# Optimization experiments

Hardware: AMD Instinct MI355X
Metric: run time of the kernel (lower is better)

Reference implementation:

```python
import jax, jax.numpy as jnp
import numpy as np

N_NODES = 20000
N_EDGES = 320000
IN_DIM = 256
HIDDEN = 256
OUT_DIM = 128
N_LAYERS = 3
N_GROUPS = 4
EXP_PER_GROUP = 2
N_EXPERTS = N_GROUPS * EXP_PER_GROUP
TOP_K = 2


def setup_inputs() -> dict:
    key = jax.random.key(0)
    ks = jax.random.split(key, 12)
    d = HIDDEN
    r = 2 * d  # router/expert input dim: concat(node, neighbor-mean)
    x = jax.random.normal(ks[0], (N_NODES, IN_DIM), dtype=jnp.float32)
    edge_index = jax.random.randint(ks[1], (2, N_EDGES), 0, N_NODES, dtype=jnp.int32)
    s = 0.05
    Wg = jax.random.normal(ks[2], (N_LAYERS, r, N_GROUPS), dtype=jnp.float32) * s
    We = jax.random.normal(ks[3], (N_LAYERS, r, N_EXPERTS), dtype=jnp.float32) * s
    Ww = jax.random.normal(ks[4], (N_LAYERS, r, d), dtype=jnp.float32) * s
    W1 = jax.random.normal(ks[5], (N_LAYERS, N_EXPERTS, r, d), dtype=jnp.float32) * s
    b1 = jnp.zeros((N_LAYERS, N_EXPERTS, d), dtype=jnp.float32)
    W2 = jax.random.normal(ks[6], (N_LAYERS, N_EXPERTS, d, d), dtype=jnp.float32) * s
    b2 = jnp.zeros((N_LAYERS, N_EXPERTS, d), dtype=jnp.float32)
    wc = jax.random.normal(ks[7], (N_LAYERS, r, 1), dtype=jnp.float32) * s
    Wout = jax.random.normal(ks[8], (d, OUT_DIM), dtype=jnp.float32) * s
    return {"x": x, "edge_index": edge_index, "Wg": Wg, "We": We, "Ww": Ww,
            "W1": W1, "b1": b1, "W2": W2, "b2": b2, "wc": wc, "Wout": Wout}


def _moe_layer(h, src, dst, deg, Wg, We, Ww, W1, b1, W2, b2, wc):
    N = h.shape[0]
    # graph message passing: mean aggregation over incoming edges
    agg = jax.ops.segment_sum(h[src], dst, num_segments=N) / deg  # [N, d]
    r = jnp.concatenate([h, agg], axis=-1)  # [N, 2d] combined router input
    # hierarchical routing: group softmax x within-group expert softmax
    gp = jax.nn.softmax(r @ Wg, axis=-1)                                # [N, G]
    ep = jax.nn.softmax((r @ We).reshape(N, N_GROUPS, EXP_PER_GROUP), axis=-1)
    probs = (gp[..., None] * ep).reshape(N, N_EXPERTS)                  # [N, E]
    # top-k gating, renormalized
    topv, topi = jax.lax.top_k(probs, TOP_K)
    gates = jnp.zeros_like(probs).at[jnp.arange(N)[:, None], topi].set(topv)
    gates = gates / (gates.sum(-1, keepdims=True) + 1e-9)              # [N, E]
    # strong experts: per-expert 2-layer MLP, combined by gates
    hid = jax.nn.relu(jnp.einsum('nf,efd->ned', r, W1) + b1[None])      # [N, E, d]
    exp_out = jnp.einsum('ned,edo->neo', hid, W2) + b2[None]            # [N, E, d]
    strong = jnp.einsum('ne,neo->no', gates, exp_out)                   # [N, d]
    # weak shared expert + confidence gate blend
    weak = r @ Ww                                                       # [N, d]
    conf = jax.nn.sigmoid(r @ wc)                                       # [N, 1]
    return jax.nn.relu(conf * strong + (1.0 - conf) * weak)


def reference(x, edge_index, Wg, We, Ww, W1, b1, W2, b2, wc, Wout):
    src, dst = edge_index[0], edge_index[1]
    N = x.shape[0]
    deg = jax.ops.segment_sum(jnp.ones((edge_index.shape[1],), jnp.float32), dst,
                              num_segments=N)
    deg = jnp.maximum(deg, 1.0)[:, None]
    h = x
    for l in range(Wg.shape[0]):  # small fixed layer loop
        h = _moe_layer(h, src, dst, deg, Wg[l], We[l], Ww[l],
                       W1[l], b1[l], W2[l], b2[l], wc[l])
    return h @ Wout
```

## Files before the change

### kernel.cpp

```cpp
#include <hip/hip_runtime.h>

#define NN 20000
#define NEDGE 320000
#define D 256
#define RD 512
#define OD 128
#define NEXP 8
#define NSLOT (2*NN)
#define NODE_BLOCKS 79
#define ASSIGN_BLOCKS 157
#define EXP_BLOCKS 640

typedef unsigned short u16;
typedef __attribute__((ext_vector_type(4))) short short4v;
typedef __attribute__((ext_vector_type(8))) short short8v;
typedef __attribute__((ext_vector_type(16))) float f32x16;

__device__ __forceinline__ void split1(float v, u16& h, u16& m, u16& l) {
    unsigned b = __float_as_uint(v);
    h = (u16)(b >> 16);
    float fh = __uint_as_float(b & 0xffff0000u);
    float r1 = v - fh;
    unsigned b1 = __float_as_uint(r1);
    m = (u16)(b1 >> 16);
    float fm = __uint_as_float(b1 & 0xffff0000u);
    float r2 = r1 - fm;
    l = (u16)(__float_as_uint(r2) >> 16);
}


__global__ void copy_x_zero_cnt_k(const float* __restrict__ x, float* __restrict__ r,
                                  int* __restrict__ cnt) {
    int gid = blockIdx.x * 256 + threadIdx.x;
    int n = gid >> 6;
    int c4 = gid & 63;
    if (gid < NN * (D / 4)) {
        float4 v = reinterpret_cast<const float4*>(x)[gid];
        reinterpret_cast<float4*>(r + (size_t)n * RD)[c4] = v;
    }
    if (gid < NN) cnt[gid] = 0;
}

__global__ void count_edges_k(const int* __restrict__ dst, int* __restrict__ cnt) {
    int e = blockIdx.x * 256 + threadIdx.x;
    if (e < NEDGE) atomicAdd(&cnt[dst[e]], 1);
}

__global__ void block_sums_k(const int* __restrict__ cnt, int* __restrict__ bsum) {
    __shared__ int s[256];
    int i = blockIdx.x * 256 + threadIdx.x;
    s[threadIdx.x] = (i < NN) ? cnt[i] : 0;
    __syncthreads();
    for (int off = 128; off > 0; off >>= 1) {
        if (threadIdx.x < off) s[threadIdx.x] += s[threadIdx.x + off];
        __syncthreads();
    }
    if (threadIdx.x == 0) bsum[blockIdx.x] = s[0];
}

__global__ void scan_bsums_k(int* __restrict__ bsum, int* __restrict__ row_start) {
    if (blockIdx.x == 0 && threadIdx.x == 0) {
        int acc = 0;
        for (int i = 0; i < NODE_BLOCKS; i++) { int t = bsum[i]; bsum[i] = acc; acc += t; }
        row_start[NN] = acc;
    }
}

__global__ void block_scan_k(const int* __restrict__ cnt, const int* __restrict__ bsum,
                             int* __restrict__ row_start, int* __restrict__ cur) {
    __shared__ int s[256];
    int i = blockIdx.x * 256 + threadIdx.x;
    int v = (i < NN) ? cnt[i] : 0;
    s[threadIdx.x] = v;
    __syncthreads();
    for (int off = 1; off < 256; off <<= 1) {
        int t = (threadIdx.x >= off) ? s[threadIdx.x - off] : 0;
        __syncthreads();
        s[threadIdx.x] += t;
        __syncthreads();
    }
    int excl = s[threadIdx.x] - v + bsum[blockIdx.x];
    if (i < NN) { row_start[i] = excl; cur[i] = excl; }
}

__global__ void fill_csr_k(const int* __restrict__ src, const int* __restrict__ dst,
                           int* __restrict__ cur, int* __restrict__ csr_src) {
    int e = blockIdx.x * 256 + threadIdx.x;
    if (e < NEDGE) {
        int pos = atomicAdd(&cur[dst[e]], 1);
        csr_src[pos] = src[e];
    }
}

__global__ void zero_k(float* __restrict__ p, int n4) {
    int i = blockIdx.x * 256 + threadIdx.x;
    if (i < n4) reinterpret_cast<float4*>(p)[i] = make_float4(0.f, 0.f, 0.f, 0.f);
}

__global__ void aggregate_k(float* __restrict__ r, const int* __restrict__ row_start,
                            const int* __restrict__ csr_src) {
    int wid = blockIdx.x * 4 + (threadIdx.x >> 6);
    int lane = threadIdx.x & 63;
    if (wid >= NN) return;
    int beg = row_start[wid], end = row_start[wid + 1];
    float ax = 0.f, ay = 0.f, az = 0.f, aw = 0.f;
    for (int j = beg; j < end; j++) {
        int s = csr_src[j];
        float4 v = reinterpret_cast<const float4*>(r + (size_t)s * RD)[lane];
        ax += v.x; ay += v.y; az += v.z; aw += v.w;
    }
    float deg = (float)((end - beg) > 1 ? (end - beg) : 1);
    float4 o = make_float4(ax / deg, ay / deg, az / deg, aw / deg);
    reinterpret_cast<float4*>(r + (size_t)wid * RD + D)[lane] = o;
}

__global__ void router_k(const float* __restrict__ r, const float* __restrict__ Wg,
                         const float* __restrict__ We, const float* __restrict__ wc,
                         int* __restrict__ node_top, float* __restrict__ node_gate,
                         float* __restrict__ conf) {
    int wid = blockIdx.x * 4 + (threadIdx.x >> 6);
    int lane = threadIdx.x & 63;
    if (wid >= NN) return;

    const float* rrow = r + (size_t)wid * RD;
    float pg[4] = {0, 0, 0, 0};
    float pe[8] = {0, 0, 0, 0, 0, 0, 0, 0};
    float pc = 0.f;
#pragma unroll
    for (int i = 0; i < 8; i++) {
        int k = lane + i * 64;
        float rv = rrow[k];
        float4 wg = *reinterpret_cast<const float4*>(Wg + (size_t)k * 4);
        pg[0] = fmaf(rv, wg.x, pg[0]); pg[1] = fmaf(rv, wg.y, pg[1]);
        pg[2] = fmaf(rv, wg.z, pg[2]); pg[3] = fmaf(rv, wg.w, pg[3]);
        float4 w0 = *reinterpret_cast<const float4*>(We + (size_t)k * 8);
        float4 w1 = *reinterpret_cast<const float4*>(We + (size_t)k * 8 + 4);
        pe[0] = fmaf(rv, w0.x, pe[0]); pe[1] = fmaf(rv, w0.y, pe[1]);
        pe[2] = fmaf(rv, w0.z, pe[2]); pe[3] = fmaf(rv, w0.w, pe[3]);
        pe[4] = fmaf(rv, w1.x, pe[4]); pe[5] = fmaf(rv, w1.y, pe[5]);
        pe[6] = fmaf(rv, w1.z, pe[6]); pe[7] = fmaf(rv, w1.w, pe[7]);
        pc = fmaf(rv, wc[k], pc);
    }
#pragma unroll
    for (int off = 32; off > 0; off >>= 1) {
#pragma unroll
        for (int g = 0; g < 4; g++) pg[g] += __shfl_xor(pg[g], off);
#pragma unroll
        for (int g = 0; g < 8; g++) pe[g] += __shfl_xor(pe[g], off);
        pc += __shfl_xor(pc, off);
    }

    if (lane == 0) {
        float m = fmaxf(fmaxf(pg[0], pg[1]), fmaxf(pg[2], pg[3]));
        float eg[4]; float sg = 0.f;
#pragma unroll
        for (int g = 0; g < 4; g++) { eg[g] = expf(pg[g] - m); sg += eg[g]; }
        float probs[8];
#pragma unroll
        for (int g = 0; g < 4; g++) {
            float a = pe[2 * g], b = pe[2 * g + 1];
            float mm = fmaxf(a, b);
            float ea = expf(a - mm), eb = expf(b - mm);
            float inv = 1.f / (ea + eb);
            float gp = eg[g] / sg;
            probs[2 * g]     = gp * ea * inv;
            probs[2 * g + 1] = gp * eb * inv;
        }
        int i0 = 0; float v0 = probs[0];
#pragma unroll
        for (int j = 1; j < 8; j++) if (probs[j] > v0) { v0 = probs[j]; i0 = j; }
        int i1 = -1; float v1 = -1e30f;
#pragma unroll
        for (int j = 0; j < 8; j++) if (j != i0 && probs[j] > v1) { v1 = probs[j]; i1 = j; }
        float s = v0 + v1 + 1e-9f;
        node_top[2 * wid] = i0;  node_top[2 * wid + 1] = i1;
        node_gate[2 * wid] = v0 / s;  node_gate[2 * wid + 1] = v1 / s;
        conf[wid] = 1.f / (1.f + expf(-pc));
    }
}

__global__ void hist_part_k(const int* __restrict__ node_top, int* __restrict__ part) {
    __shared__ int h[NEXP];
    if (threadIdx.x < NEXP) h[threadIdx.x] = 0;
    __syncthreads();
    int i = blockIdx.x * 256 + threadIdx.x;
    if (i < NSLOT) atomicAdd(&h[node_top[i]], 1);
    __syncthreads();
    if (threadIdx.x < NEXP) part[blockIdx.x * NEXP + threadIdx.x] = h[threadIdx.x];
}

__global__ void scan2_k(const int* __restrict__ part, int* __restrict__ es,
                        int* __restrict__ ecur) {
    __shared__ int tot[NEXP];
    if (threadIdx.x < NEXP) {
        int s = 0;
        for (int b = 0; b < ASSIGN_BLOCKS; b++) s += part[b * NEXP + threadIdx.x];
        tot[threadIdx.x] = s;
        ecur[threadIdx.x] = 0;
    }
    __syncthreads();
    if (threadIdx.x == 0) {
        int acc = 0;
        for (int e = 0; e < NEXP; e++) { es[e] = acc; acc += tot[e]; }
        es[NEXP] = acc;
    }
}

__global__ void fill_experts_k(const int* __restrict__ node_top, const float* __restrict__ node_gate,
                               const int* __restrict__ es, int* __restrict__ ecur,
                               int* __restrict__ slot_node, float* __restrict__ slot_gate) {
    __shared__ int hcnt[NEXP], hbase[NEXP];
    int tid = threadIdx.x;
    if (tid < NEXP) hcnt[tid] = 0;
    __syncthreads();
    int i = blockIdx.x * 256 + tid;
    int e = 0, local = 0;
    bool act = (i < NSLOT);
    if (act) {
        e = node_top[i];
        local = atomicAdd(&hcnt[e], 1);
    }
    __syncthreads();
    if (tid < NEXP) hbase[tid] = (hcnt[tid] > 0) ? atomicAdd(&ecur[tid], hcnt[tid]) : 0;
    __syncthreads();
    if (act) {
        int slot = es[e] + hbase[e] + local;
        slot_node[slot] = i >> 1;
        slot_gate[slot] = node_gate[i];
    }
}

__global__ void combine_k(const float* __restrict__ strong, const float* __restrict__ weak,
                          const float* __restrict__ conf, float* __restrict__ r) {
    int gid = blockIdx.x * 256 + threadIdx.x;
    if (gid >= NN * (D / 4)) return;
    int n = gid >> 6, c4 = gid & 63;
    float4 e = reinterpret_cast<const float4*>(strong + (size_t)n * D)[c4];
    float4 w = reinterpret_cast<const float4*>(weak + (size_t)n * D)[c4];
    float cf = conf[n], cg = 1.f - cf;
    float4 o;
    o.x = fmaxf(cf * e.x + cg * w.x, 0.f);
    o.y = fmaxf(cf * e.y + cg * w.y, 0.f);
    o.z = fmaxf(cf * e.z + cg * w.z, 0.f);
    o.w = fmaxf(cf * e.w + cg * w.w, 0.f);
    reinterpret_cast<float4*>(r + (size_t)n * RD)[c4] = o;
}

__device__ __forceinline__ void btile_one(const float* __restrict__ src,
                                          u16* __restrict__ dH, u16* __restrict__ dM,
                                          u16* __restrict__ dL, int K, int N, int gid) {
    int l = gid & 63;
    int tile = gid >> 6;
    int K16 = K >> 4;
    int kb = tile % K16;
    int t2 = tile / K16;
    int N32 = N >> 5;
    int nb = t2 % N32;
    int mat = t2 / N32;
    int kbase = (kb << 4) + ((l >> 5) << 3);
    int n = (nb << 5) + (l & 31);
    const float* s = src + ((size_t)mat * K + kbase) * N + n;
    short8v vh, vm, vl;
#pragma unroll
    for (int j = 0; j < 8; j++) {
        u16 hh, mm, ll;
        split1(s[(size_t)j * N], hh, mm, ll);
        vh[j] = (short)hh; vm[j] = (short)mm; vl[j] = (short)ll;
    }
    size_t o = (size_t)gid * 8;
    *reinterpret_cast<short8v*>(dH + o) = vh;
    *reinterpret_cast<short8v*>(dM + o) = vm;
    *reinterpret_cast<short8v*>(dL + o) = vl;
}

__global__ void btile_k(const float* __restrict__ src, u16* __restrict__ dH,
                        u16* __restrict__ dM, u16* __restrict__ dL,
                        int K, int N, int total) {
    int gid = blockIdx.x * 256 + threadIdx.x;
    if (gid >= total) return;
    btile_one(src, dH, dM, dL, K, N, gid);
}

__global__ void btile3_k(const float* __restrict__ s1, u16* __restrict__ aH,
                         u16* __restrict__ aM, u16* __restrict__ aL,
                         const float* __restrict__ s2, u16* __restrict__ bH,
                         u16* __restrict__ bM, u16* __restrict__ bL,
                         const float* __restrict__ s3, u16* __restrict__ cH,
                         u16* __restrict__ cM, u16* __restrict__ cL) {
    int gid = blockIdx.x * 256 + threadIdx.x;
    if (gid < 131072) {
        btile_one(s1, aH, aM, aL, RD, D, gid);
    } else if (gid < 131072 + 65536) {
        btile_one(s2, bH, bM, bL, D, D, gid - 131072);
    } else if (gid < 131072 + 65536 + 16384) {
        btile_one(s3, cH, cM, cL, RD, D, gid - 131072 - 65536);
    }
}

template <int MODE>
__global__ __launch_bounds__(256, 5) void gemm_mfma(
    const float* __restrict__ A, int lda,
    const u16* __restrict__ BH, const u16* __restrict__ BM,
    const u16* __restrict__ BL,
    const float* __restrict__ bias,
    float* __restrict__ C, int ldc,
    const int* __restrict__ es,
    const int* __restrict__ slot_node,
    const float* __restrict__ slot_gate,
    int M, int N, int K,
    const u16* __restrict__ VH, const u16* __restrict__ VM,
    const u16* __restrict__ VL, float* __restrict__ Cw,
    int weak_base, int Mw) {
    constexpr int PL2 = 1024;
    __shared__ u16 sA[3 * PL2];

    int tid = threadIdx.x;
    int row0, valid_rows;
    bool isweak = false;
    if (MODE == 0) {
        row0 = blockIdx.x * 64;
        valid_rows = M - row0; if (valid_rows > 64) valid_rows = 64;
    } else if (MODE == 1 && (int)blockIdx.x >= weak_base) {
        isweak = true;
        row0 = ((int)blockIdx.x - weak_base) * 64;
        valid_rows = Mw - row0; if (valid_rows > 64) valid_rows = 64;
        if (valid_rows <= 0) return;
        BH = VH; BM = VM; BL = VL;
        C = Cw;
    } else {
        int bx = blockIdx.x, acc0 = 0, expert = -1, mt = 0;
        row0 = 0; valid_rows = 0;
        for (int e = 0; e < NEXP; e++) {
            int c = es[e + 1] - es[e];
            int t = (c + 63) >> 6;
            if (bx < acc0 + t) {
                expert = e; mt = bx - acc0; row0 = es[e] + (mt << 6);
                valid_rows = c - (mt << 6); if (valid_rows > 64) valid_rows = 64;
                break;
            }
            acc0 += t;
        }
        if (expert < 0) return;
        int bo = expert * N * K;
        BH += bo; BM += bo; BL += bo;
        bias += expert * D;
    }
    int ncol0 = blockIdx.y * 128;

    int srow = tid >> 2;
    int koff = (tid & 3) * 4;
    int grow;
    {
        int i0 = row0 + srow;
        if (MODE == 1 && !isweak) {
            i0 = i0 < NSLOT ? i0 : NSLOT - 1;
            grow = slot_node[i0];
        } else if (MODE == 2) {
            grow = i0 < M ? i0 : M - 1;
        } else if (MODE == 1) {
            grow = i0 < Mw ? i0 : Mw - 1;
        } else {
            grow = i0 < M ? i0 : M - 1;
        }
    }
    const float* pA = A + (size_t)grow * lda + koff;
    int woff = ((srow >> 5) * 2 + (koff >> 3)) * 256 + (srow & 31) * 8 + (koff & 4);

    int lane = tid & 63;
    int wave = tid >> 6;
    int wr = (wave & 1) * 32;
    int wc = (wave >> 1) * 64;
    int fl = lane & 31;
    int K16 = K >> 4;
    int nb0 = (ncol0 + wc) >> 5;
    int tbase0 = nb0 * K16 * 512 + lane * 8;
    int tbase1 = (nb0 + 1) * K16 * 512 + lane * 8;
    int roff = ((wr >> 5) * 2 + (lane >> 5)) * 256 + fl * 8;

    f32x16 acc0 = {};
    f32x16 acc1 = {};

    for (int kt = 0; kt < K; kt += 16) {
        float4 av = *reinterpret_cast<const float4*>(pA + kt);
        int ko = (kt >> 4) * 512;
        short8v bH0 = *reinterpret_cast<const short8v*>(BH + tbase0 + ko);
        short8v bM0 = *reinterpret_cast<const short8v*>(BM + tbase0 + ko);
        short8v bL0 = *reinterpret_cast<const short8v*>(BL + tbase0 + ko);
        short8v bH1 = *reinterpret_cast<const short8v*>(BH + tbase1 + ko);
        short8v bM1 = *reinterpret_cast<const short8v*>(BM + tbase1 + ko);
        short8v bL1 = *reinterpret_cast<const short8v*>(BL + tbase1 + ko);
        __syncthreads();
        {
            u16 h0, m0, l0, h1, m1, l1, h2, m2, l2, h3, m3, l3;
            split1(av.x, h0, m0, l0);
            split1(av.y, h1, m1, l1);
            split1(av.z, h2, m2, l2);
            split1(av.w, h3, m3, l3);
            short4v hv = {(short)h0, (short)h1, (short)h2, (short)h3};
            short4v mv = {(short)m0, (short)m1, (short)m2, (short)m3};
            short4v lv = {(short)l0, (short)l1, (short)l2, (short)l3};
            *reinterpret_cast<short4v*>(&sA[0 * PL2 + woff]) = hv;
            *reinterpret_cast<short4v*>(&sA[1 * PL2 + woff]) = mv;
            *reinterpret_cast<short4v*>(&sA[2 * PL2 + woff]) = lv;
        }
        __syncthreads();
        short8v aH = *reinterpret_cast<const short8v*>(&sA[0 * PL2 + roff]);
        short8v aM = *reinterpret_cast<const short8v*>(&sA[1 * PL2 + roff]);
        short8v aL = *reinterpret_cast<const short8v*>(&sA[2 * PL2 + roff]);
#define MFMA_ACC(d, a, b) d = __builtin_amdgcn_mfma_f32_32x32x16_bf16(a, b, d, 0, 0, 0)
        MFMA_ACC(acc0, aH, bH0); MFMA_ACC(acc0, aH, bM0);
        MFMA_ACC(acc0, aM, bH0); MFMA_ACC(acc0, aH, bL0);
        MFMA_ACC(acc0, aM, bM0); MFMA_ACC(acc0, aL, bH0);
        MFMA_ACC(acc1, aH, bH1); MFMA_ACC(acc1, aH, bM1);
        MFMA_ACC(acc1, aM, bH1); MFMA_ACC(acc1, aH, bL1);
        MFMA_ACC(acc1, aM, bM1); MFMA_ACC(acc1, aL, bH1);
#undef MFMA_ACC
    }

    int fh = lane >> 5;
#pragma unroll
    for (int j = 0; j < 2; j++) {
        const f32x16& a = j ? acc1 : acc0;
        int colg = ncol0 + wc + j * 32 + fl;
        float bv = (MODE != 0 && !isweak) ? bias[colg] : 0.f;
#pragma unroll
        for (int rg = 0; rg < 16; rg++) {
            int lrow = wr + (rg & 3) + 8 * (rg >> 2) + 4 * fh;
            if (lrow >= valid_rows) continue;
            int growo = row0 + lrow;
            float v = a[rg] + bv;
            if (MODE == 1 && !isweak) {
                v = fmaxf(v, 0.f);
                C[(size_t)growo * ldc + colg] = v;
            } else if (MODE == 2) {
                v *= slot_gate[growo];
                int node = slot_node[growo];
                atomicAdd(&C[(size_t)node * ldc + colg], v);
            } else {
                C[(size_t)growo * ldc + colg] = v;
            }
        }
    }
}

extern "C" void kernel_launch(void* const* d_in, const int* in_sizes, int n_in,
                              void* d_out, int out_size, void* d_ws, size_t ws_size,
                              hipStream_t stream) {
    (void)in_sizes; (void)n_in; (void)out_size; (void)ws_size;
    const float* x    = (const float*)d_in[0];
    const int*   ei   = (const int*)d_in[1];
    const float* Wg   = (const float*)d_in[2];
    const float* We   = (const float*)d_in[3];
    const float* Ww   = (const float*)d_in[4];
    const float* W1   = (const float*)d_in[5];
    const float* b1   = (const float*)d_in[6];
    const float* W2   = (const float*)d_in[7];
    const float* b2   = (const float*)d_in[8];
    const float* wcp  = (const float*)d_in[9];
    const float* Wout = (const float*)d_in[10];
    float* out = (float*)d_out;

    char* p = (char*)d_ws;
    auto alloc = [&](size_t bytes) -> char* {
        char* q = p; p += (bytes + 255) & ~(size_t)255; return q;
    };
    int*   cnt       = (int*)alloc((size_t)NN * 4);
    int*   row_start = (int*)alloc((size_t)(NN + 1) * 4);
    int*   cur       = (int*)alloc((size_t)NN * 4);
    int*   bsum      = (int*)alloc(128 * 4);
    int*   csr_src   = (int*)alloc((size_t)NEDGE * 4);
    float* r         = (float*)alloc((size_t)NN * RD * 4);
    float* hid       = (float*)alloc((size_t)NSLOT * D * 4);
    float* strong    = (float*)alloc((size_t)NN * D * 4);
    float* weak      = (float*)alloc((size_t)NN * D * 4);
    float* conf      = (float*)alloc((size_t)NN * 4);
    int*   node_top  = (int*)alloc((size_t)2 * NN * 4);
    float* node_gate = (float*)alloc((size_t)2 * NN * 4);
    int*   slot_node = (int*)alloc((size_t)NSLOT * 4);
    float* slot_gate = (float*)alloc((size_t)NSLOT * 4);
    int*   part      = (int*)alloc((size_t)ASSIGN_BLOCKS * NEXP * 4);
    int*   es        = (int*)alloc(64 * 4);
    int*   ecur      = (int*)alloc(64 * 4);
    u16* w1tH = (u16*)alloc((size_t)NEXP * D * RD * 2);
    u16* w1tM = (u16*)alloc((size_t)NEXP * D * RD * 2);
    u16* w1tL = (u16*)alloc((size_t)NEXP * D * RD * 2);
    u16* w2tH = (u16*)alloc((size_t)NEXP * D * D * 2);
    u16* w2tM = (u16*)alloc((size_t)NEXP * D * D * 2);
    u16* w2tL = (u16*)alloc((size_t)NEXP * D * D * 2);
    u16* wwtH = (u16*)alloc((size_t)D * RD * 2);
    u16* wwtM = (u16*)alloc((size_t)D * RD * 2);
    u16* wwtL = (u16*)alloc((size_t)D * RD * 2);
    u16* wotH = (u16*)alloc((size_t)OD * D * 2);
    u16* wotM = (u16*)alloc((size_t)OD * D * 2);
    u16* wotL = (u16*)alloc((size_t)OD * D * 2);

    const int* srcp = ei;
    const int* dstp = ei + NEDGE;
    const int EB = (NEDGE + 255) / 256;

    copy_x_zero_cnt_k<<<5000, 256, 0, stream>>>(x, r, cnt);
    count_edges_k<<<EB, 256, 0, stream>>>(dstp, cnt);
    block_sums_k<<<NODE_BLOCKS, 256, 0, stream>>>(cnt, bsum);
    scan_bsums_k<<<1, 64, 0, stream>>>(bsum, row_start);
    block_scan_k<<<NODE_BLOCKS, 256, 0, stream>>>(cnt, bsum, row_start, cur);
    fill_csr_k<<<EB, 256, 0, stream>>>(srcp, dstp, cur, csr_src);
    btile_k<<<16, 256, 0, stream>>>(Wout, wotH, wotM, wotL, D, OD, 4096);

    for (int l = 0; l < 3; l++) {
        btile3_k<<<832, 256, 0, stream>>>(
            W1 + (size_t)l * NEXP * RD * D, w1tH, w1tM, w1tL,
            W2 + (size_t)l * NEXP * D * D,  w2tH, w2tM, w2tL,
            Ww + (size_t)l * RD * D,        wwtH, wwtM, wwtL);
        aggregate_k<<<5000, 256, 0, stream>>>(r, row_start, csr_src);
        router_k<<<5000, 256, 0, stream>>>(r,
            Wg + (size_t)l * RD * 4, We + (size_t)l * RD * 8, wcp + (size_t)l * RD,
            node_top, node_gate, conf);
        hist_part_k<<<ASSIGN_BLOCKS, 256, 0, stream>>>(node_top, part);
        scan2_k<<<1, 64, 0, stream>>>(part, es, ecur);
        fill_experts_k<<<ASSIGN_BLOCKS, 256, 0, stream>>>(node_top, node_gate, es, ecur,
                                                          slot_node, slot_gate);
        zero_k<<<5000, 256, 0, stream>>>(strong, NN * D / 4);
        gemm_mfma<1><<<dim3(EXP_BLOCKS + 313, 2), 256, 0, stream>>>(
            r, RD, w1tH, w1tM, w1tL, b1 + (size_t)l * NEXP * D, hid, D,
            es, slot_node, slot_gate, NSLOT, D, RD,
            wwtH, wwtM, wwtL, weak, EXP_BLOCKS, NN);
        gemm_mfma<2><<<dim3(EXP_BLOCKS, 2), 256, 0, stream>>>(
            hid, D, w2tH, w2tM, w2tL, b2 + (size_t)l * NEXP * D, strong, D,
            es, slot_node, slot_gate, NSLOT, D, D,
            nullptr, nullptr, nullptr, nullptr, 1 << 30, 0);
        combine_k<<<5000, 256, 0, stream>>>(strong, weak, conf, r);
    }
    gemm_mfma<0><<<dim3(313, 1), 256, 0, stream>>>(
        r, RD, wotH, wotM, wotL, nullptr, out, OD,
        nullptr, nullptr, nullptr, NN, OD, D,
        nullptr, nullptr, nullptr, nullptr, 1 << 30, 0);
}
```

Before: 859.8 us.

## Replace atomic scatter of expert outputs with per-slot stores and gather in combine

The second expert GEMM now writes gated outputs to a per-slot buffer with plain stores instead of atomically adding into a per-node strong buffer. fill_experts records each node's two slot indices, and combine_k gathers and sums the two slot rows. This removes the per-layer zeroing kernel and the float atomics, and makes the summation order deterministic. The cost is a larger intermediate buffer and two indirect reads per node in combine.

```diff
diff --git a/kernel.cpp b/kernel.cpp
--- a/kernel.cpp
+++ b/kernel.cpp
@@ -90,11 +90,6 @@
         int pos = atomicAdd(&cur[dst[e]], 1);
         csr_src[pos] = src[e];
     }
-}
-
-__global__ void zero_k(float* __restrict__ p, int n4) {
-    int i = blockIdx.x * 256 + threadIdx.x;
-    if (i < n4) reinterpret_cast<float4*>(p)[i] = make_float4(0.f, 0.f, 0.f, 0.f);
 }
 
 __global__ void aggregate_k(float* __restrict__ r, const int* __restrict__ row_start,
@@ -208,7 +203,8 @@
 
 __global__ void fill_experts_k(const int* __restrict__ node_top, const float* __restrict__ node_gate,
                                const int* __restrict__ es, int* __restrict__ ecur,
-                               int* __restrict__ slot_node, float* __restrict__ slot_gate) {
+                               int* __restrict__ slot_node, float* __restrict__ slot_gate,
+                               int* __restrict__ node_slot) {
     __shared__ int hcnt[NEXP], hbase[NEXP];
     int tid = threadIdx.x;
     if (tid < NEXP) hcnt[tid] = 0;
@@ -227,22 +223,26 @@
         int slot = es[e] + hbase[e] + local;
         slot_node[slot] = i >> 1;
         slot_gate[slot] = node_gate[i];
-    }
-}
-
-__global__ void combine_k(const float* __restrict__ strong, const float* __restrict__ weak,
-                          const float* __restrict__ conf, float* __restrict__ r) {
+        node_slot[i] = slot;
+    }
+}
+
+__global__ void combine_k(const float* __restrict__ expout, const float* __restrict__ weak,
+                          const float* __restrict__ conf, const int* __restrict__ node_slot,
+                          float* __restrict__ r) {
     int gid = blockIdx.x * 256 + threadIdx.x;
     if (gid >= NN * (D / 4)) return;
     int n = gid >> 6, c4 = gid & 63;
-    float4 e = reinterpret_cast<const float4*>(strong + (size_t)n * D)[c4];
-    float4 w = reinterpret_cast<const float4*>(weak + (size_t)n * D)[c4];
+    int s0 = node_slot[2 * n], s1 = node_slot[2 * n + 1];
+    float4 e0 = reinterpret_cast<const float4*>(expout + (size_t)s0 * D)[c4];
+    float4 e1 = reinterpret_cast<const float4*>(expout + (size_t)s1 * D)[c4];
+    float4 w  = reinterpret_cast<const float4*>(weak + (size_t)n * D)[c4];
     float cf = conf[n], cg = 1.f - cf;
     float4 o;
-    o.x = fmaxf(cf * e.x + cg * w.x, 0.f);
-    o.y = fmaxf(cf * e.y + cg * w.y, 0.f);
-    o.z = fmaxf(cf * e.z + cg * w.z, 0.f);
-    o.w = fmaxf(cf * e.w + cg * w.w, 0.f);
+    o.x = fmaxf(cf * (e0.x + e1.x) + cg * w.x, 0.f);
+    o.y = fmaxf(cf * (e0.y + e1.y) + cg * w.y, 0.f);
+    o.z = fmaxf(cf * (e0.z + e1.z) + cg * w.z, 0.f);
+    o.w = fmaxf(cf * (e0.w + e1.w) + cg * w.w, 0.f);
     reinterpret_cast<float4*>(r + (size_t)n * RD)[c4] = o;
 }
 
@@ -431,14 +431,10 @@
             float v = a[rg] + bv;
             if (MODE == 1 && !isweak) {
                 v = fmaxf(v, 0.f);
-                C[(size_t)growo * ldc + colg] = v;
             } else if (MODE == 2) {
                 v *= slot_gate[growo];
-                int node = slot_node[growo];
-                atomicAdd(&C[(size_t)node * ldc + colg], v);
-            } else {
-                C[(size_t)growo * ldc + colg] = v;
             }
+            C[(size_t)growo * ldc + colg] = v;
         }
     }
 }
@@ -471,11 +467,12 @@
     int*   csr_src   = (int*)alloc((size_t)NEDGE * 4);
     float* r         = (float*)alloc((size_t)NN * RD * 4);
     float* hid       = (float*)alloc((size_t)NSLOT * D * 4);
-    float* strong    = (float*)alloc((size_t)NN * D * 4);
+    float* expout    = (float*)alloc((size_t)NSLOT * D * 4);
     float* weak      = (float*)alloc((size_t)NN * D * 4);
     float* conf      = (float*)alloc((size_t)NN * 4);
     int*   node_top  = (int*)alloc((size_t)2 * NN * 4);
     float* node_gate = (float*)alloc((size_t)2 * NN * 4);
+    int*   node_slot = (int*)alloc((size_t)2 * NN * 4);
     int*   slot_node = (int*)alloc((size_t)NSLOT * 4);
     float* slot_gate = (float*)alloc((size_t)NSLOT * 4);
     int*   part      = (int*)alloc((size_t)ASSIGN_BLOCKS * NEXP * 4);
@@ -518,17 +515,16 @@
         hist_part_k<<<ASSIGN_BLOCKS, 256, 0, stream>>>(node_top, part);
         scan2_k<<<1, 64, 0, stream>>>(part, es, ecur);
         fill_experts_k<<<ASSIGN_BLOCKS, 256, 0, stream>>>(node_top, node_gate, es, ecur,
-                                                          slot_node, slot_gate);
-        zero_k<<<5000, 256, 0, stream>>>(strong, NN * D / 4);
+                                                          slot_node, slot_gate, node_slot);
         gemm_mfma<1><<<dim3(EXP_BLOCKS + 313, 2), 256, 0, stream>>>(
             r, RD, w1tH, w1tM, w1tL, b1 + (size_t)l * NEXP * D, hid, D,
             es, slot_node, slot_gate, NSLOT, D, RD,
             wwtH, wwtM, wwtL, weak, EXP_BLOCKS, NN);
         gemm_mfma<2><<<dim3(EXP_BLOCKS, 2), 256, 0, stream>>>(
-            hid, D, w2tH, w2tM, w2tL, b2 + (size_t)l * NEXP * D, strong, D,
+            hid, D, w2tH, w2tM, w2tL, b2 + (size_t)l * NEXP * D, expout, D,
             es, slot_node, slot_gate, NSLOT, D, D,
             nullptr, nullptr, nullptr, nullptr, 1 << 30, 0);
-        combine_k<<<5000, 256, 0, stream>>>(strong, weak, conf, r);
+        combine_k<<<5000, 256, 0, stream>>>(expout, weak, conf, node_slot, r);
     }
     gemm_mfma<0><<<dim3(313, 1), 256, 0, stream>>>(
         r, RD, wotH, wotM, wotL, nullptr, out, OD,
```

Result: faster. 813.5 us (-5.4%).
